# Kernel tuning notes

Hardware: AMD Instinct MI355X
Metric: run time of the kernel (lower is better)

The kernel has to match this reference:

```python
import jax, jax.numpy as jnp
import numpy as np

N_NODES = 100000
N_EDGES = 1600000
IN_DIM = 256
HID = 128
R = 3  # num_relations


def layer_norm(h, gamma, beta, eps=1e-5):
    mu = h.mean(axis=-1, keepdims=True)
    var = ((h - mu) ** 2).mean(axis=-1, keepdims=True)
    return (h - mu) * jax.lax.rsqrt(var + eps) * gamma + beta


def rgcn_conv(h, src, dst, etype, W, root, bias):
    """PyG RGCNConv with aggr='mean'. W:[R,in,out], root:[in,out], bias:[out]."""
    N = h.shape[0]
    out_dim = W.shape[-1]
    trans = jnp.einsum('ni,rio->rno', h, W)            # [R, N, out]
    msgs = trans[etype, src]                            # [E, out] gather per edge
    seg = dst * R + etype                               # combined (node, relation) segment id
    sums = jax.ops.segment_sum(msgs, seg, num_segments=N * R)          # [N*R, out]
    cnt = jax.ops.segment_sum(jnp.ones_like(msgs[:, 0]), seg, num_segments=N * R)
    agg = (sums / jnp.maximum(cnt, 1.0)[:, None]).reshape(N, R, out_dim).sum(axis=1)
    return agg + h @ root + bias


def setup_inputs() -> dict:
    key = jax.random.key(0)
    ks = jax.random.split(key, 10)
    s = lambda *sh: 1.0 / np.sqrt(sh[-2])
    inp = {
        'x': jax.random.normal(ks[0], (N_NODES, IN_DIM), dtype=jnp.float32),
        'edge_index': jax.random.randint(ks[1], (2, N_EDGES), 0, N_NODES, dtype=jnp.int64),
        'edge_type': jax.random.randint(ks[2], (N_EDGES,), 0, R, dtype=jnp.int64),
        # layer 0: in=256 -> out=128
        'W0': jax.random.normal(ks[3], (R, IN_DIM, HID), dtype=jnp.float32) / np.sqrt(IN_DIM),
        'root0': jax.random.normal(ks[4], (IN_DIM, HID), dtype=jnp.float32) / np.sqrt(IN_DIM),
        'b0': jnp.zeros((HID,), dtype=jnp.float32),
        'g0': jnp.ones((HID,), dtype=jnp.float32),
        'be0': jnp.zeros((HID,), dtype=jnp.float32),
        # layer 1: in=128 -> out=128
        'W1': jax.random.normal(ks[5], (R, HID, HID), dtype=jnp.float32) / np.sqrt(HID),
        'root1': jax.random.normal(ks[6], (HID, HID), dtype=jnp.float32) / np.sqrt(HID),
        'b1': jnp.zeros((HID,), dtype=jnp.float32),
        'g1': jnp.ones((HID,), dtype=jnp.float32),
        'be1': jnp.zeros((HID,), dtype=jnp.float32),
        # output LayerNorm (projection is Identity since hidden==output)
        'gout': jnp.ones((HID,), dtype=jnp.float32),
        'bout': jnp.zeros((HID,), dtype=jnp.float32),
    }
    return inp


def reference(x, edge_index, edge_type, W0, root0, b0, g0, be0,
              W1, root1, b1, g1, be1, gout, bout):
    src, dst = edge_index[0], edge_index[1]
    h = rgcn_conv(x, src, dst, edge_type, W0, root0, b0)
    h = layer_norm(h, g0, be0)
    h = jax.nn.leaky_relu(h, negative_slope=0.2)  # dropout = identity (eval)
    h = rgcn_conv(h, src, dst, edge_type, W1, root1, b1)
    h = layer_norm(h, g1, be1)
    h = layer_norm(h, gout, bout)  # output_projection is Identity
    return h
```

## Files before the change

kernel.cpp:

```cpp
#include <hip/hip_runtime.h>

#define NN 100000
#define EE 1600000

#define FB2  1568
#define NR   12500
#define GBX  782
#define GB0  (GBX * 4)
#define PB0  512
#define PB1  256
#define CVB  2048

typedef unsigned short ushortT;
typedef unsigned int uintT;
typedef __attribute__((ext_vector_type(4))) float f32x4;
typedef __attribute__((ext_vector_type(8))) short bf16x8;

__device__ inline float bf2f(ushortT b) {
    return __uint_as_float(((uintT)b) << 16);
}
__device__ inline ushortT f2bf(float f) {
    uintT u = __float_as_uint(f);
    u += 0x7FFFu + ((u >> 16) & 1u);
    return (ushortT)(u >> 16);
}

__device__ inline void gload_lds16(const void* g, void* l) {
    __builtin_amdgcn_global_load_lds((const __attribute__((address_space(1))) void*)g,
                                     (__attribute__((address_space(3))) void*)l, 16, 0, 0);
}

__device__ void cvt_role(int bid, const float* __restrict__ x, ushortT* __restrict__ xb) {
    const int total = NN * 256 / 4;
    for (int i = bid * 256 + threadIdx.x; i < total; i += CVB * 256) {
        float4 v = ((const float4*)x)[i];
        ushort4 o;
        o.x = f2bf(v.x); o.y = f2bf(v.y); o.z = f2bf(v.z); o.w = f2bf(v.w);
        ((ushort4*)xb)[i] = o;
    }
}

template <int K>
__device__ void bpack_role(int bid, const float* __restrict__ W,
                           const float* __restrict__ root, ushortT* __restrict__ Bpack) {
    constexpr int KB = K / 32;
    int idx = bid * 256 + threadIdx.x;
    if (idx >= 512 * K) return;
    int j = idx & 7;
    int l = (idx >> 3) & 63;
    int blk = idx >> 9;
    int kb = blk % KB, nblk = blk / KB;
    int k = kb * 32 + (l >> 4) * 8 + j;
    int m = nblk * 16 + (l & 15);
    float v;
    if (m < 384) {
        v = W[(((size_t)(m >> 7)) * K + k) * 128 + (m & 127)];
    } else {
        v = root[(size_t)k * 128 + (m - 384)];
    }
    Bpack[idx] = f2bf(v);
}

__global__ __launch_bounds__(256) void fill_kernel(const int* __restrict__ esrc,
                                                   const int* __restrict__ edst,
                                                   const int* __restrict__ etyp,
                                                   uintT* __restrict__ cursor,
                                                   uintT* __restrict__ elist) {
    const int bid = blockIdx.x;
    const int g = bid & 7;
    const int j = bid >> 3;
    const int lo = g * NR, hi = lo + NR;
    const int base = j * 8192;
    for (int k0 = 0; k0 < 8192; k0 += 1024) {
        int e0 = base + k0 + threadIdx.x;
        int d[4];
#pragma unroll
        for (int t = 0; t < 4; ++t) {
            int e = e0 + t * 256;
            d[t] = (e < EE) ? __builtin_nontemporal_load(&edst[e]) : -1;
        }
#pragma unroll
        for (int t = 0; t < 4; ++t) {
            if (d[t] >= lo && d[t] < hi) {
                int e = e0 + t * 256;
                int s = __builtin_nontemporal_load(&esrc[e]);
                int r = __builtin_nontemporal_load(&etyp[e]);
                if ((unsigned)s < NN && (unsigned)r < 3u) {
                    uintT add = 1u + (r == 1 ? (1u << 10) : 0u) + (r == 2 ? (1u << 20) : 0u);
                    uintT old = atomicAdd(&cursor[d[t]], add);
                    uintT pos = old & 1023u;
                    if (pos < 64u) elist[(size_t)d[t] * 64 + pos] = ((uintT)s << 2) | (uintT)r;
                }
            }
        }
    }
}

__device__ inline int swz_off(int r, int g) {
    return r * 32 + ((g ^ ((r >> 1) & 3)) << 3);
}

template <int K>
__device__ void gemm_role(int bx, int by, const ushortT* __restrict__ A,
                          const ushortT* __restrict__ Bpack, ushortT* __restrict__ C,
                          int N, ushortT* As ) {
    constexpr int KB = K / 32;
    const int tid = threadIdx.x;
    const int lane = tid & 63;
    const int wid = tid >> 6;
    const int wr = wid >> 1, wc = wid & 1;
    const int bm = bx * 128;
    const int bnblk = by * 8;

    size_t src_off[2];
#pragma unroll
    for (int t = 0; t < 2; ++t) {
        int U = (wid * 2 + t) * 64 + lane;
        int r = U >> 2;
        int g = (U & 3) ^ ((r >> 1) & 3);
        int row = bm + r;
        if (row > N - 1) row = N - 1;
        src_off[t] = (size_t)row * K + g * 8;
    }

    auto stage_issue = [&](int kblk, int buf) {
#pragma unroll
        for (int t = 0; t < 2; ++t)
            gload_lds16(&A[src_off[t] + kblk * 32], &As[buf * 4096 + (wid * 2 + t) * 512]);
    };
    f32x4 acc[4][4] = {};
    bf16x8 breg[4], bnext[4];
    auto load_b = [&](int kblk, bf16x8* out) {
#pragma unroll
        for (int nb = 0; nb < 4; ++nb) {
            int nblk = bnblk + wc * 4 + nb;
            out[nb] = *(const bf16x8*)&Bpack[((size_t)(nblk * KB + kblk) * 64 + lane) * 8];
        }
    };

    stage_issue(0, 0);
    load_b(0, breg);

    for (int kblk = 0; kblk < KB; ++kblk) {
        const int cur = kblk & 1;
        __syncthreads();
        if (kblk + 1 < KB) stage_issue(kblk + 1, cur ^ 1);
        bf16x8 afrag[4];
#pragma unroll
        for (int mb = 0; mb < 4; ++mb) {
            int fr = wr * 64 + mb * 16 + (lane & 15);
            afrag[mb] = *(const bf16x8*)&As[cur * 4096 + swz_off(fr, lane >> 4)];
        }
        if (kblk + 1 < KB) load_b(kblk + 1, bnext);
#pragma unroll
        for (int mb = 0; mb < 4; ++mb)
#pragma unroll
            for (int nb = 0; nb < 4; ++nb)
                acc[mb][nb] = __builtin_amdgcn_mfma_f32_16x16x32_bf16(
                    afrag[mb], breg[nb], acc[mb][nb], 0, 0, 0);
        if (kblk + 1 < KB) {
#pragma unroll
            for (int nb = 0; nb < 4; ++nb) breg[nb] = bnext[nb];
        }
    }

#pragma unroll
    for (int mb = 0; mb < 4; ++mb) {
        int row0 = bm + wr * 64 + mb * 16 + ((lane >> 4) << 2);
#pragma unroll
        for (int nb = 0; nb < 4; ++nb) {
            int col = (bnblk + wc * 4 + nb) * 16 + (lane & 15);
#pragma unroll
            for (int q = 0; q < 4; ++q) {
                int row = row0 + q;
                if (row < N) C[(size_t)row * 512 + col] = f2bf(acc[mb][nb][q]);
            }
        }
    }
}

__global__ __launch_bounds__(256) void k1_kernel(const float* __restrict__ x,
                                                 ushortT* __restrict__ xb,
                                                 const float* __restrict__ W0,
                                                 const float* __restrict__ root0,
                                                 ushortT* __restrict__ Bpack0,
                                                 const float* __restrict__ W1,
                                                 const float* __restrict__ root1,
                                                 ushortT* __restrict__ Bpack1) {
    int bid = blockIdx.x;
    if (bid < CVB) { cvt_role(bid, x, xb); return; }
    bid -= CVB;
    if (bid < PB0) { bpack_role<256>(bid, W0, root0, Bpack0); return; }
    bid -= PB0;
    bpack_role<128>(bid, W1, root1, Bpack1);
}

__global__ __launch_bounds__(256) void gemm0_kernel(const ushortT* __restrict__ A,
                                                    const ushortT* __restrict__ Bpack,
                                                    ushortT* __restrict__ C) {
    __shared__ ushortT As[2 * 4096];
    gemm_role<256>(blockIdx.x % GBX, blockIdx.x / GBX, A, Bpack, C, NN, As);
}

__global__ __launch_bounds__(256) void gemm1_kernel(const ushortT* __restrict__ A,
                                                    const ushortT* __restrict__ Bpack,
                                                    ushortT* __restrict__ C) {
    __shared__ ushortT As[2 * 4096];
    gemm_role<128>(blockIdx.x % GBX, blockIdx.x / GBX, A, Bpack, C, NN, As);
}

template <int LAYER>
__global__ __launch_bounds__(256) void agg_finalize_kernel(
    const ushortT* __restrict__ trans, const uintT* __restrict__ elist,
    const uintT* __restrict__ cursor,
    const float* __restrict__ bias, const float* __restrict__ gamma,
    const float* __restrict__ beta, const float* __restrict__ gout,
    const float* __restrict__ bout, void* __restrict__ outp) {
    const int wid = threadIdx.x >> 6;
    const int lane = threadIdx.x & 63;
    const int n = blockIdx.x * 4 + wid;
    const int c2 = lane * 2;
    const int cbyte = c2 * 2;

    const uintT cw = cursor[n];
    const int deg = (int)(cw & 1023u);
    const int cr1 = (int)((cw >> 10) & 1023u);
    const int cr2 = (int)((cw >> 20) & 1023u);
    const int cr0 = deg - cr1 - cr2;
    const float i0 = 1.0f / fmaxf((float)cr0, 1.0f);
    const float i1 = 1.0f / fmaxf((float)cr1, 1.0f);
    const float i2 = 1.0f / fmaxf((float)cr2, 1.0f);
    const char* tb = (const char*)trans;
    const uintT* el = elist + (size_t)n * 64;

    float p0 = 0.f, p1 = 0.f, q0 = 0.f, q1 = 0.f;
    float r0a = 0.f, r1a = 0.f, s0a = 0.f, s1a = 0.f;

    if (deg > 0) {
        int idx0 = lane & 7;
        uintT evv = el[idx0 < deg ? idx0 : deg - 1];
        for (int i = 0; i < deg; i += 8) {
            uintT evn = 0;
            if (i + 8 < deg) {
                int idx = i + 8 + (lane & 7);
                evn = el[idx < deg ? idx : deg - 1];
            }
#pragma unroll
            for (int k = 0; k < 8; ++k) {
                uintT ev = (uintT)__builtin_amdgcn_readlane((int)evv, k);
                uintT off = (ev >> 2) * 1024u + (ev & 3u) * 256u;
                ushort2 u = *(const ushort2*)(tb + off + cbyte);
                int r = (int)(ev & 3u);
                float wr_ = r == 0 ? i0 : (r == 1 ? i1 : i2);
                float w = (i + k < deg) ? wr_ : 0.f;
                float f0 = w * bf2f(u.x), f1 = w * bf2f(u.y);
                if ((k & 3) == 0) { p0 += f0; p1 += f1; }
                else if ((k & 3) == 1) { q0 += f0; q1 += f1; }
                else if ((k & 3) == 2) { r0a += f0; r1a += f1; }
                else { s0a += f0; s1a += f1; }
            }
            evv = evn;
        }
    }
    float a0 = (p0 + q0) + (r0a + s0a);
    float a1 = (p1 + q1) + (r1a + s1a);

    ushort2 rt = *(const ushort2*)&trans[(size_t)n * 512 + 384 + c2];
    float v0 = a0 + bf2f(rt.x) + bias[c2 + 0];
    float v1 = a1 + bf2f(rt.y) + bias[c2 + 1];

    float s = v0 + v1, s2 = v0 * v0 + v1 * v1;
#pragma unroll
    for (int m = 32; m >= 1; m >>= 1) {
        s += __shfl_xor(s, m);
        s2 += __shfl_xor(s2, m);
    }
    float mu = s * (1.0f / 128.0f);
    float rstd = rsqrtf(s2 * (1.0f / 128.0f) - mu * mu + 1e-5f);
    float y0 = (v0 - mu) * rstd * gamma[c2 + 0] + beta[c2 + 0];
    float y1 = (v1 - mu) * rstd * gamma[c2 + 1] + beta[c2 + 1];

    if (LAYER == 0) {
        y0 = y0 > 0.f ? y0 : 0.2f * y0;
        y1 = y1 > 0.f ? y1 : 0.2f * y1;
        ushort2 o;
        o.x = f2bf(y0);
        o.y = f2bf(y1);
        *(ushort2*)&((ushortT*)outp)[(size_t)n * 128 + c2] = o;
    } else {
        float t = y0 + y1, t2 = y0 * y0 + y1 * y1;
#pragma unroll
        for (int m = 32; m >= 1; m >>= 1) {
            t += __shfl_xor(t, m);
            t2 += __shfl_xor(t2, m);
        }
        float mu2 = t * (1.0f / 128.0f);
        float rstd2 = rsqrtf(t2 * (1.0f / 128.0f) - mu2 * mu2 + 1e-5f);
        float2 o;
        o.x = (y0 - mu2) * rstd2 * gout[c2 + 0] + bout[c2 + 0];
        o.y = (y1 - mu2) * rstd2 * gout[c2 + 1] + bout[c2 + 1];
        *(float2*)&((float*)outp)[(size_t)n * 128 + c2] = o;
    }
}

extern "C" void kernel_launch(void* const* d_in, const int* in_sizes, int n_in,
                              void* d_out, int out_size, void* d_ws, size_t ws_size,
                              hipStream_t stream) {
    const float* x     = (const float*)d_in[0];
    const int*   eidx  = (const int*)d_in[1];
    const int*   etyp  = (const int*)d_in[2];
    const float* W0    = (const float*)d_in[3];
    const float* root0 = (const float*)d_in[4];
    const float* b0    = (const float*)d_in[5];
    const float* g0    = (const float*)d_in[6];
    const float* be0   = (const float*)d_in[7];
    const float* W1    = (const float*)d_in[8];
    const float* root1 = (const float*)d_in[9];
    const float* b1    = (const float*)d_in[10];
    const float* g1    = (const float*)d_in[11];
    const float* be1   = (const float*)d_in[12];
    const float* gout  = (const float*)d_in[13];
    const float* bout  = (const float*)d_in[14];

    const int* esrc = eidx;
    const int* edst = eidx + EE;

    const size_t sz_trans  = (size_t)NN * 512 * 2;
    const size_t sz_h1     = (size_t)NN * 128 * 2;
    const size_t sz_bpack0 = (size_t)512 * 256 * 2;
    const size_t sz_bpack1 = (size_t)512 * 128 * 2;
    const size_t sz_xb     = (size_t)NN * 256 * 2;
    const size_t sz_cur    = (size_t)NN * 4;
    const size_t sz_elist  = (size_t)NN * 64 * 4;
    if (ws_size < sz_trans + sz_h1 + sz_bpack0 + sz_bpack1 + sz_xb + sz_cur + sz_elist)
        return;

    char* ws = (char*)d_ws;
    ushortT* trans  = (ushortT*)ws; ws += sz_trans;
    ushortT* h1     = (ushortT*)ws; ws += sz_h1;
    ushortT* Bpack0 = (ushortT*)ws; ws += sz_bpack0;
    ushortT* Bpack1 = (ushortT*)ws; ws += sz_bpack1;
    ushortT* xb     = (ushortT*)ws; ws += sz_xb;
    uintT*   cursor = (uintT*)ws;   ws += sz_cur;
    uintT*   elist  = (uintT*)ws;   ws += sz_elist;

    hipMemsetAsync(cursor, 0, sz_cur, stream);

    fill_kernel<<<FB2, 256, 0, stream>>>(esrc, edst, etyp, cursor, elist);

    k1_kernel<<<CVB + PB0 + PB1, 256, 0, stream>>>(x, xb, W0, root0, Bpack0,
                                                   W1, root1, Bpack1);

    gemm0_kernel<<<GB0, 256, 0, stream>>>(xb, Bpack0, trans);
    agg_finalize_kernel<0><<<NN / 4, 256, 0, stream>>>(trans, elist, cursor, b0, g0, be0,
                                                       nullptr, nullptr, h1);

    gemm1_kernel<<<GB0, 256, 0, stream>>>(h1, Bpack1, trans);
    agg_finalize_kernel<1><<<NN / 4, 256, 0, stream>>>(trans, elist, cursor, b1, g1, be1,
                                                       gout, bout, d_out);
}
```

Measured before the change: 379.4 us.

## Merge edge fill into prep kernel and remap GEMM blocks per XCD

Folds the edge-bucketing fill kernel into the same launch as the bf16 conversion and weight packing, so those independent jobs run concurrently and one launch goes away. The GEMM grid is remapped so the four column tiles of a row block land on the same XCD, which should improve L2 reuse of the A rows. The grid is padded to 3136 blocks with early exits for the extras. It also clamps the degree used in aggregation to the 64-entry edge list capacity, a small correctness guard.

Result: faster. 342.3 us, median of 2 (-9.8%).

```diff
diff --git a/kernel.cpp b/kernel.cpp
--- a/kernel.cpp
+++ b/kernel.cpp
@@ -6,7 +6,7 @@
 #define FB2  1568
 #define NR   12500
 #define GBX  782
-#define GB0  (GBX * 4)
+#define GBS  3136
 #define PB0  512
 #define PB1  256
 #define CVB  2048
@@ -61,12 +61,9 @@
     Bpack[idx] = f2bf(v);
 }
 
-__global__ __launch_bounds__(256) void fill_kernel(const int* __restrict__ esrc,
-                                                   const int* __restrict__ edst,
-                                                   const int* __restrict__ etyp,
-                                                   uintT* __restrict__ cursor,
-                                                   uintT* __restrict__ elist) {
-    const int bid = blockIdx.x;
+__device__ void fill_role(int bid, const int* __restrict__ esrc,
+                          const int* __restrict__ edst, const int* __restrict__ etyp,
+                          uintT* __restrict__ cursor, uintT* __restrict__ elist) {
     const int g = bid & 7;
     const int j = bid >> 3;
     const int lo = g * NR, hi = lo + NR;
@@ -96,6 +93,23 @@
     }
 }
 
+__global__ __launch_bounds__(256) void k1_kernel(
+    const int* __restrict__ esrc, const int* __restrict__ edst,
+    const int* __restrict__ etyp, uintT* __restrict__ cursor, uintT* __restrict__ elist,
+    const float* __restrict__ x, ushortT* __restrict__ xb,
+    const float* __restrict__ W0, const float* __restrict__ root0,
+    ushortT* __restrict__ Bpack0, const float* __restrict__ W1,
+    const float* __restrict__ root1, ushortT* __restrict__ Bpack1) {
+    int bid = blockIdx.x;
+    if (bid < FB2) { fill_role(bid, esrc, edst, etyp, cursor, elist); return; }
+    bid -= FB2;
+    if (bid < CVB) { cvt_role(bid, x, xb); return; }
+    bid -= CVB;
+    if (bid < PB0) { bpack_role<256>(bid, W0, root0, Bpack0); return; }
+    bid -= PB0;
+    bpack_role<128>(bid, W1, root1, Bpack1);
+}
+
 __device__ inline int swz_off(int r, int g) {
     return r * 32 + ((g ^ ((r >> 1) & 3)) << 3);
 }
@@ -179,34 +193,30 @@
     }
 }
 
-__global__ __launch_bounds__(256) void k1_kernel(const float* __restrict__ x,
-                                                 ushortT* __restrict__ xb,
-                                                 const float* __restrict__ W0,
-                                                 const float* __restrict__ root0,
-                                                 ushortT* __restrict__ Bpack0,
-                                                 const float* __restrict__ W1,
-                                                 const float* __restrict__ root1,
-                                                 ushortT* __restrict__ Bpack1) {
-    int bid = blockIdx.x;
-    if (bid < CVB) { cvt_role(bid, x, xb); return; }
-    bid -= CVB;
-    if (bid < PB0) { bpack_role<256>(bid, W0, root0, Bpack0); return; }
-    bid -= PB0;
-    bpack_role<128>(bid, W1, root1, Bpack1);
+template <int K>
+__device__ void gemm_dispatch(const ushortT* A, const ushortT* Bpack, ushortT* C,
+                              ushortT* As) {
+    const int bid = blockIdx.x;
+    const int xcd = bid & 7;
+    const int slot = bid >> 3;
+    const int bx = xcd + 8 * (slot >> 2);
+    const int by = slot & 3;
+    if (bx >= GBX) return;
+    gemm_role<K>(bx, by, A, Bpack, C, NN, As);
 }
 
 __global__ __launch_bounds__(256) void gemm0_kernel(const ushortT* __restrict__ A,
                                                     const ushortT* __restrict__ Bpack,
                                                     ushortT* __restrict__ C) {
     __shared__ ushortT As[2 * 4096];
-    gemm_role<256>(blockIdx.x % GBX, blockIdx.x / GBX, A, Bpack, C, NN, As);
+    gemm_dispatch<256>(A, Bpack, C, As);
 }
 
 __global__ __launch_bounds__(256) void gemm1_kernel(const ushortT* __restrict__ A,
                                                     const ushortT* __restrict__ Bpack,
                                                     ushortT* __restrict__ C) {
     __shared__ ushortT As[2 * 4096];
-    gemm_role<128>(blockIdx.x % GBX, blockIdx.x / GBX, A, Bpack, C, NN, As);
+    gemm_dispatch<128>(A, Bpack, C, As);
 }
 
 template <int LAYER>
@@ -223,13 +233,14 @@
     const int cbyte = c2 * 2;
 
     const uintT cw = cursor[n];
-    const int deg = (int)(cw & 1023u);
+    int deg = (int)(cw & 1023u);
     const int cr1 = (int)((cw >> 10) & 1023u);
     const int cr2 = (int)((cw >> 20) & 1023u);
     const int cr0 = deg - cr1 - cr2;
     const float i0 = 1.0f / fmaxf((float)cr0, 1.0f);
     const float i1 = 1.0f / fmaxf((float)cr1, 1.0f);
     const float i2 = 1.0f / fmaxf((float)cr2, 1.0f);
+    if (deg > 64) deg = 64;
     const char* tb = (const char*)trans;
     const uintT* el = elist + (size_t)n * 64;
 
@@ -346,16 +357,14 @@
 
     hipMemsetAsync(cursor, 0, sz_cur, stream);
 
-    fill_kernel<<<FB2, 256, 0, stream>>>(esrc, edst, etyp, cursor, elist);
-
-    k1_kernel<<<CVB + PB0 + PB1, 256, 0, stream>>>(x, xb, W0, root0, Bpack0,
-                                                   W1, root1, Bpack1);
-
-    gemm0_kernel<<<GB0, 256, 0, stream>>>(xb, Bpack0, trans);
+    k1_kernel<<<FB2 + CVB + PB0 + PB1, 256, 0, stream>>>(
+        esrc, edst, etyp, cursor, elist, x, xb, W0, root0, Bpack0, W1, root1, Bpack1);
+
+    gemm0_kernel<<<GBS, 256, 0, stream>>>(xb, Bpack0, trans);
     agg_finalize_kernel<0><<<NN / 4, 256, 0, stream>>>(trans, elist, cursor, b0, g0, be0,
                                                        nullptr, nullptr, h1);
 
-    gemm1_kernel<<<GB0, 256, 0, stream>>>(h1, Bpack1, trans);
+    gemm1_kernel<<<GBS, 256, 0, stream>>>(h1, Bpack1, trans);
     agg_finalize_kernel<1><<<NN / 4, 256, 0, stream>>>(trans, elist, cursor, b1, g1, be1,
                                                        gout, bout, d_out);
 }
```
